# Performance work log

Hardware: AMD Instinct MI355X
Metric: run time of the kernel (lower is better)

Reference implementation:

```python
import jax, jax.numpy as jnp
import numpy as np
from jax import lax

DIM, HEADS, HIDDEN = 384, 6, 1536
B, D, H, W = 2, 14, 14, 14
LN_EPS = 1e-5


def setup_inputs() -> dict:
    key = jax.random.key(0)
    ks = jax.random.split(key, 8)
    s = 0.02
    return {
        "x": jax.random.normal(ks[0], (B, DIM, D, H, W), jnp.float32),
        "conv_w": jax.random.normal(ks[1], (DIM, 1, 3, 3, 3), jnp.float32) * s,
        "conv_b": jnp.zeros((DIM,), jnp.float32),
        "ln1_w": jnp.ones((DIM,), jnp.float32),
        "ln1_b": jnp.zeros((DIM,), jnp.float32),
        "qkv_w": jax.random.normal(ks[2], (3 * DIM, DIM), jnp.float32) * s,
        "proj_w": jax.random.normal(ks[3], (DIM, DIM), jnp.float32) * s,
        "proj_b": jnp.zeros((DIM,), jnp.float32),
        "ln2_w": jnp.ones((DIM,), jnp.float32),
        "ln2_b": jnp.zeros((DIM,), jnp.float32),
        "fc1_w": jax.random.normal(ks[4], (HIDDEN, DIM), jnp.float32) * s,
        "fc1_b": jnp.zeros((HIDDEN,), jnp.float32),
        "fc2_w": jax.random.normal(ks[5], (DIM, HIDDEN), jnp.float32) * s,
        "fc2_b": jnp.zeros((DIM,), jnp.float32),
    }


def _layernorm(x, w, b):
    mu = jnp.mean(x, axis=-1, keepdims=True)
    var = jnp.var(x, axis=-1, keepdims=True)
    return (x - mu) * lax.rsqrt(var + LN_EPS) * w + b


def reference(x, conv_w, conv_b, ln1_w, ln1_b, qkv_w, proj_w, proj_b,
              ln2_w, ln2_b, fc1_w, fc1_b, fc2_w, fc2_b):
    Bn, C = x.shape[0], x.shape[1]
    Dd, Hh, Ww = x.shape[2], x.shape[3], x.shape[4]
    # depthwise conv3d positional embedding (groups=dim), padding=1
    pos = lax.conv_general_dilated(
        x, conv_w, window_strides=(1, 1, 1), padding="SAME",
        feature_group_count=C,
        dimension_numbers=("NCDHW", "OIDHW", "NCDHW"))
    x = x + pos + conv_b[None, :, None, None, None] * 0 + conv_b[None, :, None, None, None]
    # fix: bias belongs to conv output only once
    x = x - conv_b[None, :, None, None, None]
    N = Dd * Hh * Ww
    t = x.reshape(Bn, C, N).transpose(0, 2, 1)  # [B, N, C]

    # attention
    hd = C // HEADS
    scale = hd ** -0.5
    tn = _layernorm(t, ln1_w, ln1_b)
    qkv = tn @ qkv_w.T  # [B, N, 3C]
    qkv = qkv.reshape(Bn, N, 3, HEADS, hd).transpose(2, 0, 3, 1, 4)
    q, k, v = qkv[0], qkv[1], qkv[2]  # [B, H, N, hd]
    attn = jax.nn.softmax(jnp.einsum("bhnd,bhmd->bhnm", q, k) * scale, axis=-1)
    o = jnp.einsum("bhnm,bhmd->bhnd", attn, v)
    o = o.transpose(0, 2, 1, 3).reshape(Bn, N, C)
    t = t + o @ proj_w.T + proj_b

    # MLP (exact GELU, matching torch nn.GELU default)
    tn2 = _layernorm(t, ln2_w, ln2_b)
    h = jax.nn.gelu(tn2 @ fc1_w.T + fc1_b, approximate=False)
    t = t + h @ fc2_w.T + fc2_b

    return t.transpose(0, 2, 1).reshape(Bn, C, Dd, Hh, Ww)
```

## Files before the change

### kernel.cpp

```cpp
#include <hip/hip_runtime.h>
#include <hip/hip_bf16.h>
#include <math.h>

#define DIM 384
#define HEADS 6
#define HIDDEN 1536
#define NTOK 2744
#define BATCH 2
#define MTOT (BATCH * NTOK)
#define KSPLIT 4
#define NQT 11
#define CEXP 0.18033688f

typedef __bf16 bf16x8 __attribute__((ext_vector_type(8)));
typedef __bf16 bf16x4 __attribute__((ext_vector_type(4)));
typedef float  f32x4  __attribute__((ext_vector_type(4)));

#define F_GELU  1
#define F_RESID 2
#define F_BF16  4
#define F_QKV   8
#define F_TRANS 16

__device__ __forceinline__ void gll16(const void* g, void* l) {
    __builtin_amdgcn_global_load_lds(
        (const __attribute__((address_space(1))) unsigned int*)g,
        (__attribute__((address_space(3))) unsigned int*)l, 16, 0, 0);
}

__global__ void k_conv(const float* __restrict__ x, const float* __restrict__ cw,
                       float* __restrict__ t,
                       const float* __restrict__ w0, const float* __restrict__ w1,
                       const float* __restrict__ w2, const float* __restrict__ w3,
                       __bf16* o0, __bf16* o1, __bf16* o2, __bf16* o3) {
    int bid = blockIdx.x;
    if (bid >= 528) {
        int i = (bid - 528) * 256 + threadIdx.x;
        const float* s; __bf16* d; int off;
        if (i < 110592)      { s = w0; d = o0; off = i; }
        else if (i < 147456) { s = w1; d = o1; off = i - 110592; }
        else if (i < 294912) { s = w2; d = o2; off = i - 147456; }
        else                 { s = w3; d = o3; off = i - 294912; }
        float4 v = ((const float4*)s)[off];
        bf16x4 bb = { (__bf16)v.x, (__bf16)v.y, (__bf16)v.z, (__bf16)v.w };
        *(bf16x4*)(d + (size_t)off * 4) = bb;
        return;
    }
    int nb = bid % 11, rest = bid / 11;
    int cb = rest % 24, b = rest / 24;
    int c0 = cb * 16;
    int n = nb * 256 + threadIdx.x;
    if (n >= NTOK) return;
    int d = n / 196, r = n % 196, h = r / 14, w = r % 14;
    const float* xb = x + ((size_t)b * DIM + c0) * NTOK;
    float acc[16];
    #pragma unroll
    for (int c = 0; c < 16; c++) acc[c] = xb[(size_t)c * NTOK + n];
    #pragma unroll
    for (int kd = 0; kd < 3; kd++) {
        int dd = d + kd - 1;
        if (dd < 0 || dd >= 14) continue;
        #pragma unroll
        for (int kh = 0; kh < 3; kh++) {
            int hh = h + kh - 1;
            if (hh < 0 || hh >= 14) continue;
            #pragma unroll
            for (int kw = 0; kw < 3; kw++) {
                int ww = w + kw - 1;
                if (ww < 0 || ww >= 14) continue;
                int np = (dd * 14 + hh) * 14 + ww;
                int tap = kd * 9 + kh * 3 + kw;
                #pragma unroll
                for (int c = 0; c < 16; c++)
                    acc[c] = fmaf(cw[(c0 + c) * 27 + tap], xb[(size_t)c * NTOK + np], acc[c]);
            }
        }
    }
    float* tp = t + (size_t)(b * NTOK + n) * DIM + c0;
    #pragma unroll
    for (int c = 0; c < 16; c += 4) {
        float4 v = { acc[c], acc[c + 1], acc[c + 2], acc[c + 3] };
        *(float4*)(tp + c) = v;
    }
}

__device__ __forceinline__ void ln_body(const float* __restrict__ in,
                                        __bf16* __restrict__ out,
                                        const float* __restrict__ w,
                                        const float* __restrict__ b) {
    int wid = threadIdx.x >> 6, lane = threadIdx.x & 63;
    int token = blockIdx.x * 4 + wid;
    const float* row = in + (size_t)token * DIM;
    float v[6], s = 0.f, s2 = 0.f;
    #pragma unroll
    for (int i = 0; i < 6; i++) {
        v[i] = row[lane + 64 * i];
        s += v[i]; s2 += v[i] * v[i];
    }
    #pragma unroll
    for (int m = 1; m < 64; m <<= 1) { s += __shfl_xor(s, m); s2 += __shfl_xor(s2, m); }
    float mu = s * (1.f / DIM);
    float rstd = rsqrtf(s2 * (1.f / DIM) - mu * mu + 1e-5f);
    __bf16* orow = out + (size_t)token * DIM;
    #pragma unroll
    for (int i = 0; i < 6; i++) {
        int c = lane + 64 * i;
        orow[c] = (__bf16)((v[i] - mu) * rstd * w[c] + b[c]);
    }
}
__global__ void k_ln1(const float* in, __bf16* out, const float* w, const float* b) {
    ln_body(in, out, w, b);
}
__global__ void k_ln2(const float* in, __bf16* out, const float* w, const float* b) {
    ln_body(in, out, w, b);
}

__device__ __forceinline__ void gemm12864_body(
    const __bf16* __restrict__ A, const __bf16* __restrict__ B,
    const float* __restrict__ bias, void* __restrict__ out,
    __bf16* __restrict__ vt_out, int M, int N, int K, int flags) {
    __shared__ __bf16 As[128][64];
    __shared__ __bf16 Bs[64][64];
    int tid = threadIdx.x, lane = tid & 63, wid = tid >> 6;
    int quad = lane >> 4, l16 = lane & 15;
    int wm = wid & 1, wn = wid >> 1;
    int m0 = blockIdx.y * 128, n0 = blockIdx.x * 64;
    int x7 = l16 & 7;

    auto stage = [&](int k0) {
        #pragma unroll
        for (int i = 0; i < 4; i++) {
            int c = i * 256 + tid;
            int row = c >> 3, cc = (c & 7) ^ (row & 7);
            int gm = m0 + row; if (gm > M - 1) gm = M - 1;
            gll16(A + (size_t)gm * K + k0 + cc * 8, &As[0][0] + (size_t)c * 8);
        }
        #pragma unroll
        for (int i = 0; i < 2; i++) {
            int c = i * 256 + tid;
            int row = c >> 3, cc = (c & 7) ^ (row & 7);
            gll16(B + (size_t)(n0 + row) * K + k0 + cc * 8, &Bs[0][0] + (size_t)c * 8);
        }
    };

    f32x4 acc[4][2] = {};
    int nk = K >> 6;
    for (int ki = 0; ki < nk; ki++) {
        if (ki) __syncthreads();
        stage(ki << 6);
        __syncthreads();
        #pragma unroll
        for (int s = 0; s < 2; s++) {
            bf16x8 a[4], b[2];
            #pragma unroll
            for (int i = 0; i < 4; i++)
                a[i] = *(bf16x8*)&As[wm * 64 + i * 16 + l16][(((s * 4 + quad) ^ x7)) * 8];
            #pragma unroll
            for (int j = 0; j < 2; j++)
                b[j] = *(bf16x8*)&Bs[wn * 32 + j * 16 + l16][(((s * 4 + quad) ^ x7)) * 8];
            #pragma unroll
            for (int i = 0; i < 4; i++)
                #pragma unroll
                for (int j = 0; j < 2; j++)
                    acc[i][j] = __builtin_amdgcn_mfma_f32_16x16x32_bf16(a[i], b[j], acc[i][j], 0, 0, 0);
        }
    }

    int colb = n0 + wn * 32;
    #pragma unroll
    for (int j = 0; j < 2; j++) {
        int col = colb + j * 16 + l16;
        float bv = bias ? bias[col] : 0.f;
        #pragma unroll
        for (int i = 0; i < 4; i++) {
            int row0 = m0 + wm * 64 + i * 16 + quad * 4;
            if (row0 >= M) continue;
            float v4[4];
            #pragma unroll
            for (int r = 0; r < 4; r++) {
                float v = acc[i][j][r] + bv;
                if (flags & F_GELU) v = 0.5f * v * (1.f + erff(v * 0.70710678f));
                if ((flags & F_QKV) && col < 384) v *= CEXP;
                v4[r] = v;
            }
            if ((flags & F_QKV) && col >= 768) {
                int b2 = row0 / NTOK, n2 = row0 - b2 * NTOK;
                bf16x4 pk = { (__bf16)v4[0], (__bf16)v4[1], (__bf16)v4[2], (__bf16)v4[3] };
                *(bf16x4*)(vt_out + ((size_t)(b2 * DIM + (col - 768))) * NTOK + n2) = pk;
            } else {
                #pragma unroll
                for (int r = 0; r < 4; r++)
                    ((__bf16*)out)[(size_t)(row0 + r) * N + col] = (__bf16)v4[r];
            }
        }
    }
}
__global__ __launch_bounds__(256) void k_qkv(const __bf16* A, const __bf16* B,
        void* out, __bf16* vt_out, int M, int N, int K) {
    gemm12864_body(A, B, nullptr, out, vt_out, M, N, K, F_QKV);
}
__global__ __launch_bounds__(256) void k_fc1(const __bf16* A, const __bf16* B,
        const float* bias, void* out, int M, int N, int K) {
    gemm12864_body(A, B, bias, out, nullptr, M, N, K, F_GELU | F_BF16);
}

__device__ __forceinline__ void gemm64_body(
    const __bf16* __restrict__ A, const __bf16* __restrict__ B,
    const float* __restrict__ bias, const float* __restrict__ resid,
    void* __restrict__ out, int M, int N, int K, int flags) {
    __shared__ __align__(16) char sm[17408];
    __bf16 (*As)[64] = (__bf16(*)[64])sm;
    __bf16 (*Bs)[64] = (__bf16(*)[64])(sm + 8192);
    float* Tt = (float*)sm;
    int tid = threadIdx.x, lane = tid & 63, wid = tid >> 6;
    int quad = lane >> 4, l16 = lane & 15;
    int wm = wid & 1, wn = wid >> 1;
    int m0 = blockIdx.y * 64, n0 = blockIdx.x * 64;
    int x7 = l16 & 7;

    auto stage = [&](int k0) {
        #pragma unroll
        for (int i = 0; i < 2; i++) {
            int c = i * 256 + tid;
            int row = c >> 3, cc = (c & 7) ^ (row & 7);
            int gm = m0 + row; if (gm > M - 1) gm = M - 1;
            gll16(A + (size_t)gm * K + k0 + cc * 8, &As[0][0] + (size_t)c * 8);
        }
        #pragma unroll
        for (int i = 0; i < 2; i++) {
            int c = i * 256 + tid;
            int row = c >> 3, cc = (c & 7) ^ (row & 7);
            gll16(B + (size_t)(n0 + row) * K + k0 + cc * 8, &Bs[0][0] + (size_t)c * 8);
        }
    };

    f32x4 acc[2][2] = {};
    int nk = K >> 6;
    for (int ki = 0; ki < nk; ki++) {
        if (ki) __syncthreads();
        stage(ki << 6);
        __syncthreads();
        #pragma unroll
        for (int s = 0; s < 2; s++) {
            bf16x8 a[2], b[2];
            #pragma unroll
            for (int i = 0; i < 2; i++)
                a[i] = *(bf16x8*)&As[wm * 32 + i * 16 + l16][(((s * 4 + quad) ^ x7)) * 8];
            #pragma unroll
            for (int j = 0; j < 2; j++)
                b[j] = *(bf16x8*)&Bs[wn * 32 + j * 16 + l16][(((s * 4 + quad) ^ x7)) * 8];
            #pragma unroll
            for (int i = 0; i < 2; i++)
                #pragma unroll
                for (int j = 0; j < 2; j++)
                    acc[i][j] = __builtin_amdgcn_mfma_f32_16x16x32_bf16(a[i], b[j], acc[i][j], 0, 0, 0);
        }
    }

    if (flags & F_TRANS) {
        #pragma unroll
        for (int half = 0; half < 2; half++) {
            __syncthreads();
            if (wn == half) {
                #pragma unroll
                for (int j = 0; j < 2; j++) {
                    int colL = j * 16 + l16;
                    int col = n0 + half * 32 + colL;
                    float bv = bias[col];
                    #pragma unroll
                    for (int i = 0; i < 2; i++) {
                        int rowL = wm * 32 + i * 16 + quad * 4;
                        float v4[4];
                        #pragma unroll
                        for (int r = 0; r < 4; r++) {
                            int rr = m0 + rowL + r; if (rr > M - 1) rr = M - 1;
                            v4[r] = acc[i][j][r] + bv + resid[(size_t)rr * N + col];
                        }
                        float4 pk = { v4[0], v4[1], v4[2], v4[3] };
                        *(float4*)&Tt[colL * 68 + rowL] = pk;
                    }
                }
            }
            __syncthreads();
            int c = tid >> 3, no = (tid & 7) * 8;
            int col = n0 + half * 32 + c;
            #pragma unroll
            for (int q2 = 0; q2 < 2; q2++) {
                int nn = no + q2 * 4;
                int row = m0 + nn;
                if (row >= M) continue;
                int b2 = row / NTOK, n2 = row - b2 * NTOK;
                float4 v = *(float4*)&Tt[c * 68 + nn];
                *(float4*)((float*)out + ((size_t)(b2 * N + col)) * NTOK + n2) = v;
            }
        }
        return;
    }

    #pragma unroll
    for (int j = 0; j < 2; j++) {
        int col = n0 + wn * 32 + j * 16 + l16;
        float bv = bias ? bias[col] : 0.f;
        #pragma unroll
        for (int i = 0; i < 2; i++) {
            int row0 = m0 + wm * 32 + i * 16 + quad * 4;
            if (row0 >= M) continue;
            #pragma unroll
            for (int r = 0; r < 4; r++) {
                float v = acc[i][j][r] + bv;
                if (flags & F_RESID) v += resid[(size_t)(row0 + r) * N + col];
                ((float*)out)[(size_t)(row0 + r) * N + col] = v;
            }
        }
    }
}
__global__ __launch_bounds__(256) void k_proj(const __bf16* A, const __bf16* B,
        const float* bias, const float* resid, void* out, int M, int N, int K) {
    gemm64_body(A, B, bias, resid, out, M, N, K, F_RESID);
}
__global__ __launch_bounds__(256) void k_fc2(const __bf16* A, const __bf16* B,
        const float* bias, const float* resid, void* out, int M, int N, int K) {
    gemm64_body(A, B, bias, resid, out, M, N, K, F_RESID | F_TRANS);
}

__global__ __launch_bounds__(512, 4) void k_attn(const __bf16* __restrict__ qkv,
                                                 const __bf16* __restrict__ vt,
                                                 __bf16* __restrict__ opart,
                                                 float* __restrict__ lpart) {
    __shared__ __align__(16) char smemQP[256 * 64 * 2];
    __shared__ __align__(16) __bf16 Ks[2][64][64];
    __shared__ __align__(16) __bf16 Vt[2][64][64];
    __bf16 (*Qs)[64] = (__bf16(*)[64])smemQP;
    __bf16* PB = (__bf16*)smemQP;

    int tid = threadIdx.x, lane = tid & 63, wid = tid >> 6;
    int quad = lane >> 4, l16 = lane & 15;
    int q0 = blockIdx.x * 256;
    int bh = blockIdx.y;
    int ks = blockIdx.z;
    int b = bh / HEADS, h = bh % HEADS;
    int x7 = l16 & 7;

    int kt0 = (43 * ks) / KSPLIT, kt1 = (43 * (ks + 1)) / KSPLIT;

    int srow = tid >> 3, scc = (tid & 7) ^ (srow & 7);
    const __bf16* pK = qkv + ((size_t)(b * NTOK + kt0 * 64 + srow)) * 1152 + 384 + h * 64 + scc * 8;
    const __bf16* pV = vt + ((size_t)(bh * 64 + srow)) * NTOK + kt0 * 64 + scc * 8;

    auto stageKV = [&](int kt, int bufi) {
        const __bf16* kp = pK + (size_t)(kt - kt0) * (64 * 1152);
        if (kt == 42 && srow >= 56)
            kp = qkv + ((size_t)(b * NTOK + NTOK - 1)) * 1152 + 384 + h * 64 + scc * 8;
        gll16(kp, &Ks[bufi][0][0] + (size_t)tid * 8);
        gll16(pV + (size_t)(kt - kt0) * 64, &Vt[bufi][0][0] + (size_t)tid * 8);
    };

    #pragma unroll
    for (int i = 0; i < 4; i++) {
        int c = i * 512 + tid;
        int row = c >> 3, cc = (c & 7) ^ (row & 7);
        int gq = q0 + row; if (gq > NTOK - 1) gq = NTOK - 1;
        gll16(qkv + ((size_t)(b * NTOK + gq)) * 1152 + h * 64 + cc * 8,
              &Qs[0][0] + (size_t)c * 8);
    }
    stageKV(kt0, 0);
    __syncthreads();

    bf16x8 aq[2][2];
    #pragma unroll
    for (int qt = 0; qt < 2; qt++)
        #pragma unroll
        for (int s = 0; s < 2; s++)
            aq[qt][s] = *(bf16x8*)&Qs[wid * 32 + qt * 16 + l16][((s * 4 + quad) ^ x7) * 8];
    __syncthreads();

    unsigned pso[4], pro[2];
    #pragma unroll
    for (int t = 0; t < 4; t++)
        pso[t] = (unsigned)(wid * 32 + l16) * 64
               + ((unsigned)((t * 2 + (quad >> 1)) ^ x7) * 8 + (quad & 1) * 4);
    #pragma unroll
    for (int sx = 0; sx < 2; sx++)
        pro[sx] = (unsigned)(wid * 32 + l16) * 64
                + (unsigned)(((sx * 4 + quad) ^ x7) * 8);

    const f32x4 fzero = {0.f, 0.f, 0.f, 0.f};
    f32x4 oacc[2][4] = {};
    float l_lane[2] = {0.f, 0.f};

    int bufi = 0;
    for (int kt = kt0; kt < kt1; kt++) {
        if (kt > kt0) __syncthreads();
        if (kt + 1 < kt1) stageKV(kt + 1, bufi ^ 1);

        const __bf16* ksb = &Ks[bufi][0][0] + l16 * 64;
        const __bf16* vtb = &Vt[bufi][0][0] + l16 * 64;
        bool tail = (kt == 42);

        #pragma unroll
        for (int t = 0; t < 4; t++) {
            bf16x8 bk0 = *(bf16x8*)(ksb + t * 1024 + ((quad ^ x7) * 8));
            bf16x8 bk1 = *(bf16x8*)(ksb + t * 1024 + (((4 + quad) ^ x7) * 8));
            #pragma unroll
            for (int qt = 0; qt < 2; qt++) {
                f32x4 z = __builtin_amdgcn_mfma_f32_16x16x32_bf16(bk0, aq[qt][0], fzero, 0, 0, 0);
                z = __builtin_amdgcn_mfma_f32_16x16x32_bf16(bk1, aq[qt][1], z, 0, 0, 0);
                float e0 = exp2f(z[0]), e1 = exp2f(z[1]), e2 = exp2f(z[2]), e3 = exp2f(z[3]);
                if (tail) {
                    int kb = kt * 64 + t * 16 + quad * 4;
                    if (kb + 0 >= NTOK) e0 = 0.f;
                    if (kb + 1 >= NTOK) e1 = 0.f;
                    if (kb + 2 >= NTOK) e2 = 0.f;
                    if (kb + 3 >= NTOK) e3 = 0.f;
                }
                l_lane[qt] += (e0 + e1) + (e2 + e3);
                bf16x4 pk = { (__bf16)e0, (__bf16)e1, (__bf16)e2, (__bf16)e3 };
                *(bf16x4*)(PB + pso[t] + qt * 1024) = pk;
            }
        }

        bf16x8 ap[2][2];
        #pragma unroll
        for (int qt = 0; qt < 2; qt++)
            #pragma unroll
            for (int sx = 0; sx < 2; sx++)
                ap[qt][sx] = *(bf16x8*)(PB + pro[sx] + qt * 1024);

        #pragma unroll
        for (int t = 0; t < 4; t++) {
            bf16x8 bv0 = *(bf16x8*)(vtb + t * 1024 + ((quad ^ x7) * 8));
            bf16x8 bv1 = *(bf16x8*)(vtb + t * 1024 + (((4 + quad) ^ x7) * 8));
            #pragma unroll
            for (int qt = 0; qt < 2; qt++) {
                oacc[qt][t] = __builtin_amdgcn_mfma_f32_16x16x32_bf16(ap[qt][0], bv0, oacc[qt][t], 0, 0, 0);
                oacc[qt][t] = __builtin_amdgcn_mfma_f32_16x16x32_bf16(ap[qt][1], bv1, oacc[qt][t], 0, 0, 0);
            }
        }
        bufi ^= 1;
    }

    #pragma unroll
    for (int qt = 0; qt < 2; qt++) {
        float l = l_lane[qt];
        l += __shfl_xor(l, 16);
        l += __shfl_xor(l, 32);
        int gq = q0 + wid * 32 + qt * 16 + l16;
        if (quad == 0 && gq < NTOK)
            lpart[((size_t)ks * 12 + bh) * NTOK + gq] = l;
    }

    #pragma unroll
    for (int qt = 0; qt < 2; qt++)
        #pragma unroll
        for (int r = 0; r < 4; r++) {
            int gq = q0 + wid * 32 + qt * 16 + quad * 4 + r;
            if (gq >= NTOK) continue;
            __bf16* op = opart + ((size_t)ks * MTOT + (size_t)b * NTOK + gq) * DIM + h * 64;
            #pragma unroll
            for (int t = 0; t < 4; t++) op[t * 16 + l16] = (__bf16)oacc[qt][t][r];
        }
}

__global__ void k_comb(const __bf16* __restrict__ opart,
                       const float* __restrict__ lpart,
                       __bf16* __restrict__ o) {
    int idx = blockIdx.x * 256 + threadIdx.x;
    int token = idx / 96, rem = idx - token * 96;
    int c = rem * 4, h = c >> 6;
    int b2 = token / NTOK, n = token - b2 * NTOK;
    int bh = b2 * HEADS + h;
    float a0 = 0.f, a1 = 0.f, a2 = 0.f, a3 = 0.f, l = 0.f;
    #pragma unroll
    for (int ks = 0; ks < KSPLIT; ks++) {
        bf16x4 p = *(const bf16x4*)&opart[((size_t)ks * MTOT + token) * DIM + c];
        a0 += (float)p[0]; a1 += (float)p[1]; a2 += (float)p[2]; a3 += (float)p[3];
        l += lpart[((size_t)ks * 12 + bh) * NTOK + n];
    }
    float inv = 1.f / l;
    bf16x4 ov = { (__bf16)(a0 * inv), (__bf16)(a1 * inv),
                  (__bf16)(a2 * inv), (__bf16)(a3 * inv) };
    *(bf16x4*)(o + (size_t)token * DIM + c) = ov;
}

extern "C" void kernel_launch(void* const* d_in, const int* in_sizes, int n_in,
                              void* d_out, int out_size, void* d_ws, size_t ws_size,
                              hipStream_t stream) {
    const float* x      = (const float*)d_in[0];
    const float* conv_w = (const float*)d_in[1];
    const float* ln1_w  = (const float*)d_in[3];
    const float* ln1_b  = (const float*)d_in[4];
    const float* qkv_w  = (const float*)d_in[5];
    const float* proj_w = (const float*)d_in[6];
    const float* proj_b = (const float*)d_in[7];
    const float* ln2_w  = (const float*)d_in[8];
    const float* ln2_b  = (const float*)d_in[9];
    const float* fc1_w  = (const float*)d_in[10];
    const float* fc1_b  = (const float*)d_in[11];
    const float* fc2_w  = (const float*)d_in[12];
    const float* fc2_b  = (const float*)d_in[13];
    float* out = (float*)d_out;

    char* p = (char*)d_ws;
    float*  T    = (float*)p;  p += (size_t)MTOT * DIM * 4;
    __bf16* TN   = (__bf16*)p; p += (size_t)MTOT * DIM * 2;
    __bf16* QKV  = (__bf16*)p; p += (size_t)MTOT * 1152 * 2;
    __bf16* VT   = (__bf16*)p; p += (size_t)BATCH * DIM * NTOK * 2;
    __bf16* O    = (__bf16*)p; p += (size_t)MTOT * DIM * 2;
    __bf16* H    = (__bf16*)p; p += (size_t)MTOT * HIDDEN * 2;
    __bf16* WQ   = (__bf16*)p; p += (size_t)1152 * 384 * 2;
    __bf16* WP   = (__bf16*)p; p += (size_t)384 * 384 * 2;
    __bf16* W1   = (__bf16*)p; p += (size_t)1536 * 384 * 2;
    __bf16* W2   = (__bf16*)p; p += (size_t)384 * 1536 * 2;
    float*  LP   = (float*)p;  p += (size_t)KSPLIT * 12 * NTOK * 4;
    __bf16* OP   = (__bf16*)p; p += (size_t)KSPLIT * MTOT * DIM * 2;

    k_conv<<<528 + 1728, 256, 0, stream>>>(
        x, conv_w, T, qkv_w, proj_w, fc1_w, fc2_w, WQ, WP, W1, W2);
    k_ln1<<<MTOT / 4, 256, 0, stream>>>(T, TN, ln1_w, ln1_b);
    k_qkv<<<dim3(18, 43), 256, 0, stream>>>(TN, WQ, QKV, VT, MTOT, 1152, 384);
    k_attn<<<dim3(NQT, 12, KSPLIT), 512, 0, stream>>>(QKV, VT, OP, LP);
    k_comb<<<(MTOT * 96) / 256, 256, 0, stream>>>(OP, LP, O);
    k_proj<<<dim3(6, 86), 256, 0, stream>>>(O, WP, proj_b, T, T, MTOT, 384, 384);
    k_ln2<<<MTOT / 4, 256, 0, stream>>>(T, TN, ln2_w, ln2_b);
    k_fc1<<<dim3(24, 43), 256, 0, stream>>>(TN, W1, fc1_b, H, MTOT, 1536, 384);
    k_fc2<<<dim3(6, 86), 256, 0, stream>>>(H, W2, fc2_b, T, out, MTOT, 384, 1536);
}
```

Baseline: 232.7 us.

## Keep attention P in registers via transposed PV MFMA, halve query tile

The attention kernel now computes O^T = V^T·P^T, so the exponentiated score fragments feed straight into the second MFMA as register operands instead of going through an LDS round trip. Each wave handles one 16-query tile instead of two. Blocks cover 128 queries, which doubles the grid in x, and LDS shrinks to a single shared K/V double buffer that also stages Q. Launch bounds now ask for 8 blocks per CU to raise occupancy. The trade-off is that each K/V tile is reused by half as many queries, and V is read as 4-element pieces that must be reassembled into operands.

```diff
diff --git a/kernel.cpp b/kernel.cpp
--- a/kernel.cpp
+++ b/kernel.cpp
@@ -9,7 +9,7 @@
 #define BATCH 2
 #define MTOT (BATCH * NTOK)
 #define KSPLIT 4
-#define NQT 11
+#define NQT 22
 #define CEXP 0.18033688f
 
 typedef __bf16 bf16x8 __attribute__((ext_vector_type(8)));
@@ -323,19 +323,16 @@
     gemm64_body(A, B, bias, resid, out, M, N, K, F_RESID | F_TRANS);
 }
 
-__global__ __launch_bounds__(512, 4) void k_attn(const __bf16* __restrict__ qkv,
+__global__ __launch_bounds__(512, 8) void k_attn(const __bf16* __restrict__ qkv,
                                                  const __bf16* __restrict__ vt,
                                                  __bf16* __restrict__ opart,
                                                  float* __restrict__ lpart) {
-    __shared__ __align__(16) char smemQP[256 * 64 * 2];
-    __shared__ __align__(16) __bf16 Ks[2][64][64];
-    __shared__ __align__(16) __bf16 Vt[2][64][64];
-    __bf16 (*Qs)[64] = (__bf16(*)[64])smemQP;
-    __bf16* PB = (__bf16*)smemQP;
+    __shared__ __align__(16) __bf16 KV[2][2][64][64];
+    __bf16 (*Qs)[64] = (__bf16(*)[64])KV;
 
     int tid = threadIdx.x, lane = tid & 63, wid = tid >> 6;
     int quad = lane >> 4, l16 = lane & 15;
-    int q0 = blockIdx.x * 256;
+    int q0 = blockIdx.x * 128;
     int bh = blockIdx.y;
     int ks = blockIdx.z;
     int b = bh / HEADS, h = bh % HEADS;
@@ -351,114 +348,103 @@
         const __bf16* kp = pK + (size_t)(kt - kt0) * (64 * 1152);
         if (kt == 42 && srow >= 56)
             kp = qkv + ((size_t)(b * NTOK + NTOK - 1)) * 1152 + 384 + h * 64 + scc * 8;
-        gll16(kp, &Ks[bufi][0][0] + (size_t)tid * 8);
-        gll16(pV + (size_t)(kt - kt0) * 64, &Vt[bufi][0][0] + (size_t)tid * 8);
+        gll16(kp, &KV[bufi][0][0][0] + (size_t)tid * 8);
+        gll16(pV + (size_t)(kt - kt0) * 64, &KV[bufi][1][0][0] + (size_t)tid * 8);
     };
 
     #pragma unroll
-    for (int i = 0; i < 4; i++) {
+    for (int i = 0; i < 2; i++) {
         int c = i * 512 + tid;
         int row = c >> 3, cc = (c & 7) ^ (row & 7);
         int gq = q0 + row; if (gq > NTOK - 1) gq = NTOK - 1;
         gll16(qkv + ((size_t)(b * NTOK + gq)) * 1152 + h * 64 + cc * 8,
               &Qs[0][0] + (size_t)c * 8);
     }
+    __syncthreads();
+
+    bf16x8 aq[2];
+    #pragma unroll
+    for (int sx = 0; sx < 2; sx++)
+        aq[sx] = *(bf16x8*)&Qs[wid * 16 + l16][((sx * 4 + quad) ^ x7) * 8];
+    __syncthreads();
+
     stageKV(kt0, 0);
-    __syncthreads();
-
-    bf16x8 aq[2][2];
-    #pragma unroll
-    for (int qt = 0; qt < 2; qt++)
-        #pragma unroll
-        for (int s = 0; s < 2; s++)
-            aq[qt][s] = *(bf16x8*)&Qs[wid * 32 + qt * 16 + l16][((s * 4 + quad) ^ x7) * 8];
-    __syncthreads();
-
-    unsigned pso[4], pro[2];
-    #pragma unroll
-    for (int t = 0; t < 4; t++)
-        pso[t] = (unsigned)(wid * 32 + l16) * 64
-               + ((unsigned)((t * 2 + (quad >> 1)) ^ x7) * 8 + (quad & 1) * 4);
-    #pragma unroll
-    for (int sx = 0; sx < 2; sx++)
-        pro[sx] = (unsigned)(wid * 32 + l16) * 64
-                + (unsigned)(((sx * 4 + quad) ^ x7) * 8);
+
+    int koff0 = (quad ^ x7) * 8, koff1 = ((4 + quad) ^ x7) * 8;
+    int voffl[2], voffh[2];
+    #pragma unroll
+    for (int sx = 0; sx < 2; sx++) {
+        voffl[sx] = ((4 * sx + (quad >> 1)) ^ x7) * 8 + (quad & 1) * 4;
+        voffh[sx] = ((4 * sx + 2 + (quad >> 1)) ^ x7) * 8 + (quad & 1) * 4;
+    }
 
     const f32x4 fzero = {0.f, 0.f, 0.f, 0.f};
-    f32x4 oacc[2][4] = {};
-    float l_lane[2] = {0.f, 0.f};
+    f32x4 oaccT[4] = {};
+    float l_sum = 0.f;
 
     int bufi = 0;
     for (int kt = kt0; kt < kt1; kt++) {
-        if (kt > kt0) __syncthreads();
+        __syncthreads();
         if (kt + 1 < kt1) stageKV(kt + 1, bufi ^ 1);
 
-        const __bf16* ksb = &Ks[bufi][0][0] + l16 * 64;
-        const __bf16* vtb = &Vt[bufi][0][0] + l16 * 64;
+        const __bf16* ksb = &KV[bufi][0][0][0] + l16 * 64;
+        const __bf16* vtb = &KV[bufi][1][0][0] + l16 * 64;
         bool tail = (kt == 42);
 
+        bf16x8 pb[2];
         #pragma unroll
         for (int t = 0; t < 4; t++) {
-            bf16x8 bk0 = *(bf16x8*)(ksb + t * 1024 + ((quad ^ x7) * 8));
-            bf16x8 bk1 = *(bf16x8*)(ksb + t * 1024 + (((4 + quad) ^ x7) * 8));
-            #pragma unroll
-            for (int qt = 0; qt < 2; qt++) {
-                f32x4 z = __builtin_amdgcn_mfma_f32_16x16x32_bf16(bk0, aq[qt][0], fzero, 0, 0, 0);
-                z = __builtin_amdgcn_mfma_f32_16x16x32_bf16(bk1, aq[qt][1], z, 0, 0, 0);
-                float e0 = exp2f(z[0]), e1 = exp2f(z[1]), e2 = exp2f(z[2]), e3 = exp2f(z[3]);
-                if (tail) {
-                    int kb = kt * 64 + t * 16 + quad * 4;
-                    if (kb + 0 >= NTOK) e0 = 0.f;
-                    if (kb + 1 >= NTOK) e1 = 0.f;
-                    if (kb + 2 >= NTOK) e2 = 0.f;
-                    if (kb + 3 >= NTOK) e3 = 0.f;
-                }
-                l_lane[qt] += (e0 + e1) + (e2 + e3);
-                bf16x4 pk = { (__bf16)e0, (__bf16)e1, (__bf16)e2, (__bf16)e3 };
-                *(bf16x4*)(PB + pso[t] + qt * 1024) = pk;
-            }
-        }
-
-        bf16x8 ap[2][2];
-        #pragma unroll
-        for (int qt = 0; qt < 2; qt++)
-            #pragma unroll
-            for (int sx = 0; sx < 2; sx++)
-                ap[qt][sx] = *(bf16x8*)(PB + pro[sx] + qt * 1024);
-
-        #pragma unroll
-        for (int t = 0; t < 4; t++) {
-            bf16x8 bv0 = *(bf16x8*)(vtb + t * 1024 + ((quad ^ x7) * 8));
-            bf16x8 bv1 = *(bf16x8*)(vtb + t * 1024 + (((4 + quad) ^ x7) * 8));
-            #pragma unroll
-            for (int qt = 0; qt < 2; qt++) {
-                oacc[qt][t] = __builtin_amdgcn_mfma_f32_16x16x32_bf16(ap[qt][0], bv0, oacc[qt][t], 0, 0, 0);
-                oacc[qt][t] = __builtin_amdgcn_mfma_f32_16x16x32_bf16(ap[qt][1], bv1, oacc[qt][t], 0, 0, 0);
+            bf16x8 bk0 = *(bf16x8*)(ksb + t * 1024 + koff0);
+            bf16x8 bk1 = *(bf16x8*)(ksb + t * 1024 + koff1);
+            f32x4 z = __builtin_amdgcn_mfma_f32_16x16x32_bf16(bk0, aq[0], fzero, 0, 0, 0);
+            z = __builtin_amdgcn_mfma_f32_16x16x32_bf16(bk1, aq[1], z, 0, 0, 0);
+            float e0 = exp2f(z[0]), e1 = exp2f(z[1]), e2 = exp2f(z[2]), e3 = exp2f(z[3]);
+            if (tail) {
+                int kb = kt * 64 + t * 16 + quad * 4;
+                if (kb + 0 >= NTOK) e0 = 0.f;
+                if (kb + 1 >= NTOK) e1 = 0.f;
+                if (kb + 2 >= NTOK) e2 = 0.f;
+                if (kb + 3 >= NTOK) e3 = 0.f;
+            }
+            l_sum += (e0 + e1) + (e2 + e3);
+            int half = (t & 1) * 4, px = t >> 1;
+            pb[px][half + 0] = (__bf16)e0;
+            pb[px][half + 1] = (__bf16)e1;
+            pb[px][half + 2] = (__bf16)e2;
+            pb[px][half + 3] = (__bf16)e3;
+        }
+
+        #pragma unroll
+        for (int dt = 0; dt < 4; dt++) {
+            const __bf16* vr = vtb + dt * 1024;
+            #pragma unroll
+            for (int sx = 0; sx < 2; sx++) {
+                bf16x4 lo = *(bf16x4*)(vr + voffl[sx]);
+                bf16x4 hi = *(bf16x4*)(vr + voffh[sx]);
+                bf16x8 av = { lo[0], lo[1], lo[2], lo[3],
+                              hi[0], hi[1], hi[2], hi[3] };
+                oaccT[dt] = __builtin_amdgcn_mfma_f32_16x16x32_bf16(av, pb[sx], oaccT[dt], 0, 0, 0);
             }
         }
         bufi ^= 1;
     }
 
-    #pragma unroll
-    for (int qt = 0; qt < 2; qt++) {
-        float l = l_lane[qt];
-        l += __shfl_xor(l, 16);
-        l += __shfl_xor(l, 32);
-        int gq = q0 + wid * 32 + qt * 16 + l16;
-        if (quad == 0 && gq < NTOK)
-            lpart[((size_t)ks * 12 + bh) * NTOK + gq] = l;
-    }
-
-    #pragma unroll
-    for (int qt = 0; qt < 2; qt++)
-        #pragma unroll
-        for (int r = 0; r < 4; r++) {
-            int gq = q0 + wid * 32 + qt * 16 + quad * 4 + r;
-            if (gq >= NTOK) continue;
-            __bf16* op = opart + ((size_t)ks * MTOT + (size_t)b * NTOK + gq) * DIM + h * 64;
-            #pragma unroll
-            for (int t = 0; t < 4; t++) op[t * 16 + l16] = (__bf16)oacc[qt][t][r];
-        }
+    float l = l_sum;
+    l += __shfl_xor(l, 16);
+    l += __shfl_xor(l, 32);
+    int gq = q0 + wid * 16 + l16;
+    if (quad == 0 && gq < NTOK)
+        lpart[((size_t)ks * 12 + bh) * NTOK + gq] = l;
+
+    if (gq < NTOK) {
+        __bf16* op = opart + ((size_t)ks * MTOT + (size_t)b * NTOK + gq) * DIM + h * 64;
+        #pragma unroll
+        for (int dt = 0; dt < 4; dt++) {
+            bf16x4 pk = { (__bf16)oaccT[dt][0], (__bf16)oaccT[dt][1],
+                          (__bf16)oaccT[dt][2], (__bf16)oaccT[dt][3] };
+            *(bf16x4*)(op + dt * 16 + quad * 4) = pk;
+        }
+    }
 }
 
 __global__ void k_comb(const __bf16* __restrict__ opart,
```

Result: slower. 248.2 us (+6.7%).
